# Optimization experiments

Hardware: AMD Instinct MI355X
Metric: run time of the kernel (lower is better)

Reference implementation:

```python
import jax, jax.numpy as jnp
import numpy as np

N, E, B = 8192, 131072, 256
F_ATOM, D, H, HD, L, FC, BINS = 92, 256, 8, 32, 6, 512, 256
VMIN, VMAX = 0.0, 8.0


def layer_norm(x, g, b, eps=1e-5):
    mu = jnp.mean(x, axis=-1, keepdims=True)
    var = jnp.var(x, axis=-1, keepdims=True)
    return (x - mu) * jax.lax.rsqrt(var + eps) * g + b


def silu(x):
    return x * jax.nn.sigmoid(x)


def setup_inputs() -> dict:
    key = jax.random.key(0)
    ks = iter(jax.random.split(key, 80))

    def lin(fan_in, shape):
        return jax.random.normal(next(ks), shape, jnp.float32) / np.sqrt(fan_in)

    inp = {
        'x': jax.random.normal(next(ks), (N, F_ATOM), jnp.float32),
        'edge_attr': jax.random.normal(next(ks), (E, 3), jnp.float32) * 2.0,
        'edge_index': jax.random.randint(next(ks), (2, E), 0, N, dtype=jnp.int32),
        'batch': jnp.sort(jax.random.randint(next(ks), (N,), 0, B, dtype=jnp.int32)),
        # atom_embedding: Linear(92,256) -> LN -> SiLU -> Linear(256,256)
        'aw1': lin(F_ATOM, (F_ATOM, D)), 'ab1': jnp.zeros((D,)),
        'ag1': jnp.ones((D,)), 'abt1': jnp.zeros((D,)),
        'aw2': lin(D, (D, D)), 'ab2': jnp.zeros((D,)),
        # rbf MLP: Linear(256,256) LN SiLU Linear LN SiLU Linear
        'rw1': lin(BINS, (BINS, D)), 'rb1': jnp.zeros((D,)),
        'rg1': jnp.ones((D,)), 'rbt1': jnp.zeros((D,)),
        'rw2': lin(D, (D, D)), 'rb2': jnp.zeros((D,)),
        'rg2': jnp.ones((D,)), 'rbt2': jnp.zeros((D,)),
        'rw3': lin(D, (D, D)), 'rb3': jnp.zeros((D,)),
        # L stacked PrdnetConv (edge-conditioned multi-head graph attention)
        'Wq': lin(D, (L, D, D)), 'bq': jnp.zeros((L, D)),
        'Wk': lin(D, (L, D, D)), 'bk': jnp.zeros((L, D)),
        'Wv': lin(D, (L, D, D)), 'bv': jnp.zeros((L, D)),
        'We': lin(D, (L, D, D)), 'be': jnp.zeros((L, D)),
        'Wo': lin(D, (L, D, D)), 'bo': jnp.zeros((L, D)),
        'lng': jnp.ones((L, D)), 'lnb': jnp.zeros((L, D)),
        # FC head: Linear(256,512) then fc_out Linear(512,1)
        'fw1': lin(D, (D, FC)), 'fb1': jnp.zeros((FC,)),
        'fow': lin(FC, (FC, 1)), 'fob': jnp.zeros((1,)),
    }
    return inp


def _forward(x, edge_attr, edge_index, batch, aw1, ab1, ag1, abt1, aw2, ab2,
             rw1, rb1, rg1, rbt1, rw2, rb2, rg2, rbt2, rw3, rb3,
             Wq, bq, Wk, bk, Wv, bv, We, be, Wo, bo, lng, lnb,
             fw1, fb1, fow, fob):
    # atom embedding (dropout = identity at inference)
    node = silu(layer_norm(x @ aw1 + ab1, ag1, abt1)) @ aw2 + ab2  # [N, D]

    # RBF expansion of edge lengths, then edge MLP
    d = jnp.linalg.norm(edge_attr, axis=1)  # [E]
    centers = jnp.linspace(VMIN, VMAX, BINS)
    gamma = 1.0 / (centers[1] - centers[0]) ** 2
    rbf = jnp.exp(-gamma * (d[:, None] - centers[None, :]) ** 2)  # [E, BINS]
    e = silu(layer_norm(rbf @ rw1 + rb1, rg1, rbt1))
    e = silu(layer_norm(e @ rw2 + rb2, rg2, rbt2))
    e = e @ rw3 + rb3  # [E, D]

    src, dst = edge_index[0], edge_index[1]
    inv_sqrt = 1.0 / np.sqrt(HD)
    for l in range(L):
        res = node
        q = (node @ Wq[l] + bq[l]).reshape(N, H, HD)
        k = (node @ Wk[l] + bk[l]).reshape(N, H, HD)
        v = (node @ Wv[l] + bv[l]).reshape(N, H, HD)
        ee = (e @ We[l] + be[l]).reshape(E, H, HD)
        kj = k[src] + ee  # edge-conditioned keys [E, H, HD]
        vj = v[src] + ee  # edge-conditioned values
        score = jnp.sum(q[dst] * kj, axis=-1) * inv_sqrt  # [E, H]
        smax = jax.ops.segment_max(score, dst, num_segments=N)  # [N, H]
        ex = jnp.exp(score - smax[dst])
        den = jax.ops.segment_sum(ex, dst, num_segments=N)
        alpha = ex / (den[dst] + 1e-16)  # neighborhood softmax [E, H]
        msg = jax.ops.segment_sum(alpha[:, :, None] * vj, dst, num_segments=N)
        out = msg.reshape(N, D) @ Wo[l] + bo[l]
        out = layer_norm(out, lng[l], lnb[l])
        node = out + res  # residual

    # scatter-mean graph pooling
    sums = jax.ops.segment_sum(node, batch, num_segments=B)  # [B, D]
    cnt = jax.ops.segment_sum(jnp.ones((N,), node.dtype), batch, num_segments=B)
    feats = sums / jnp.clip(cnt, 1.0)[:, None]

    feats = feats @ fw1 + fb1  # single fc layer: no act (i == len-1 in source)
    return feats @ fow + fob  # [B, 1], identity link


def reference(x, edge_attr, edge_index, batch, aw1, ab1, ag1, abt1, aw2, ab2,
              rw1, rb1, rg1, rbt1, rw2, rb2, rg2, rbt2, rw3, rb3,
              Wq, bq, Wk, bk, Wv, bv, We, be, Wo, bo, lng, lnb,
              fw1, fb1, fow, fob):
    return _forward(x, edge_attr, edge_index, batch, aw1, ab1, ag1, abt1, aw2,
                    ab2, rw1, rb1, rg1, rbt1, rw2, rb2, rg2, rbt2, rw3, rb3,
                    Wq, bq, Wk, bk, Wv, bv, We, be, Wo, bo, lng, lnb,
                    fw1, fb1, fow, fob)
```

## Files before the change

kernel.cpp:

```cpp
#include <hip/hip_runtime.h>
#include <hip/hip_bf16.h>
#include <cstddef>

#define NN    8192
#define EE    131072
#define BB    256
#define F_AT  92
#define DD    256
#define HH    8
#define HDIM  32
#define LL    6
#define FCD   512

typedef __hip_bfloat16 bf16;
typedef __attribute__((ext_vector_type(8))) __bf16 bf16x8;
typedef __attribute__((ext_vector_type(4))) float f32x4;

__device__ __forceinline__ float to_f(float x) { return x; }
__device__ __forceinline__ float to_f(bf16 x) { return __bfloat162float(x); }
__device__ __forceinline__ float bfu(unsigned short u) {
    return __uint_as_float(((unsigned)u) << 16);
}
__device__ __forceinline__ unsigned short bfbits(float x) {
    bf16 h = __float2bfloat16(x);
    return *(unsigned short*)&h;
}
__device__ __forceinline__ void store_v(float* p, float v) { *p = v; }
__device__ __forceinline__ void store_v(bf16* p, float v) { *p = __float2bfloat16(v); }

__device__ __forceinline__ float4 load4(const float* p) { return *(const float4*)p; }
__device__ __forceinline__ float4 load4(const bf16* p) {
    const ushort4 r = *(const ushort4*)p;
    return make_float4(bfu(r.x), bfu(r.y), bfu(r.z), bfu(r.w));
}

__device__ __forceinline__ void store_f4(float* p, const float4& f) {
    *(float4*)p = f;
}
__device__ __forceinline__ void store_f4(bf16* p, const float4& f) {
    ushort4 u = {bfbits(f.x), bfbits(f.y), bfbits(f.z), bfbits(f.w)};
    *(ushort4*)p = u;
}

__device__ __forceinline__ bf16x8 ld8(const bf16* p) { return *(const bf16x8*)p; }
__device__ __forceinline__ bf16x8 ld8(const float* p) {
    const float4 f0 = *(const float4*)p;
    const float4 f1 = *(const float4*)(p + 4);
    bf16x8 r;
    r[0] = (__bf16)f0.x; r[1] = (__bf16)f0.y; r[2] = (__bf16)f0.z; r[3] = (__bf16)f0.w;
    r[4] = (__bf16)f1.x; r[5] = (__bf16)f1.y; r[6] = (__bf16)f1.z; r[7] = (__bf16)f1.w;
    return r;
}

__device__ __forceinline__ void async_copy16(const void* g, void* l) {
    __builtin_amdgcn_global_load_lds(
        (const __attribute__((address_space(1))) unsigned int*)g,
        (__attribute__((address_space(3))) unsigned int*)l, 16, 0, 0);
}

__global__ __launch_bounds__(256) void transpose_weights(
    const float* __restrict__ rw1, const float* __restrict__ rw2,
    const float* __restrict__ rw3, const float* __restrict__ aw2,
    const float* __restrict__ Wq, const float* __restrict__ Wk,
    const float* __restrict__ Wv, const float* __restrict__ We,
    const float* __restrict__ Wo, __bf16* __restrict__ out)
{
    __shared__ float tile[64][65];
    const int midx = blockIdx.y;
    const float* src;
    if (midx == 0) src = rw1;
    else if (midx == 1) src = rw2;
    else if (midx == 2) src = rw3;
    else if (midx == 3) src = aw2;
    else {
        const int l = (midx - 4) / 5, s = (midx - 4) % 5;
        const float* bases[5] = {Wq, Wk, Wv, We, Wo};
        src = bases[s] + (size_t)l * 65536;
    }
    __bf16* dst = out + (size_t)midx * 65536;
    const int k0 = (blockIdx.x >> 2) * 64;
    const int n0 = (blockIdx.x & 3) * 64;
    const int c = threadIdx.x & 63;
    const int r0 = threadIdx.x >> 6;
#pragma unroll
    for (int p = 0; p < 16; ++p) {
        const int r = r0 + p * 4;
        tile[r][c] = src[(size_t)(k0 + r) * 256 + n0 + c];
    }
    __syncthreads();
#pragma unroll
    for (int p = 0; p < 16; ++p) {
        const int n = r0 + p * 4;
        dst[(size_t)(n0 + n) * 256 + k0 + c] = (__bf16)tile[c][n];
    }
}

__global__ __launch_bounds__(256) void pack_qkv_bias(
    const float* __restrict__ bq, const float* __restrict__ bk,
    const float* __restrict__ bv, float* __restrict__ out)
{
    const int i = blockIdx.x * 256 + threadIdx.x;
    if (i >= LL * 768) return;
    const int l = i / 768, r = i % 768;
    const float* s = (r < 256) ? bq : (r < 512) ? bk : bv;
    out[i] = s[l * 256 + (r & 255)];
}

__global__ __launch_bounds__(256) void combine_w3e(
    const float* __restrict__ rw3, const float* __restrict__ We,
    __bf16* __restrict__ Wt_out)
{
    __shared__ float As[16][65];
    __shared__ float Ws[16][65];
    const int l = blockIdx.z;
    const float* W = We + (size_t)l * 65536;
    __bf16* dst = Wt_out + (size_t)l * 65536;
    const int m0 = blockIdx.x * 64;
    const int n0 = blockIdx.y * 64;
    const int tid = threadIdx.x;
    const int tx = tid & 15, ty = tid >> 4;
    float acc[4][4] = {};

    for (int k0 = 0; k0 < 256; k0 += 16) {
        {
            const int ar = tid >> 2;
            const int ac = (tid & 3) * 4;
#pragma unroll
            for (int j = 0; j < 4; ++j)
                As[ac + j][ar] = rw3[(size_t)(m0 + ar) * 256 + k0 + ac + j];
        }
        {
            const int wr = tid >> 4;
            const int wc = (tid & 15) * 4;
#pragma unroll
            for (int j = 0; j < 4; ++j)
                Ws[wr][wc + j] = W[(size_t)(k0 + wr) * 256 + n0 + wc + j];
        }
        __syncthreads();
#pragma unroll
        for (int kk = 0; kk < 16; ++kk) {
            float a[4], b[4];
#pragma unroll
            for (int i = 0; i < 4; ++i) a[i] = As[kk][ty * 4 + i];
#pragma unroll
            for (int j = 0; j < 4; ++j) b[j] = Ws[kk][tx * 4 + j];
#pragma unroll
            for (int i = 0; i < 4; ++i)
#pragma unroll
                for (int j = 0; j < 4; ++j) acc[i][j] += a[i] * b[j];
        }
        __syncthreads();
    }
#pragma unroll
    for (int i = 0; i < 4; ++i) {
        const int gk = m0 + ty * 4 + i;
#pragma unroll
        for (int j = 0; j < 4; ++j) {
            const int gn = n0 + tx * 4 + j;
            dst[(size_t)gn * 256 + gk] = (__bf16)acc[i][j];
        }
    }
}

__global__ __launch_bounds__(256) void combine_bias(
    const float* __restrict__ rb3, const float* __restrict__ We,
    const float* __restrict__ be, float* __restrict__ out)
{
    const int l = blockIdx.x;
    const int n = threadIdx.x;
    const float* W = We + (size_t)l * 65536;
    float s = be[l * 256 + n];
    for (int m = 0; m < 256; ++m) s += rb3[m] * W[m * 256 + n];
    out[l * 256 + n] = s;
}

__global__ __launch_bounds__(256) void mfma_gemm_ln(
    const bf16* __restrict__ A, const __bf16* __restrict__ Wt,
    const float* __restrict__ bias, const float* __restrict__ g,
    const float* __restrict__ b, bf16* __restrict__ C, int do_silu)
{
    __shared__ __align__(16) __bf16 As[64 * 64];
    __shared__ __align__(16) __bf16 Bs[256 * 64];
    const int tid = threadIdx.x;
    const int m0 = blockIdx.x * 64;
    const int wave = tid >> 6, lane = tid & 63;
    const int lm = lane & 15, lq = lane >> 4;
    const int lrow = lane >> 3;
    const int lcolsw = ((lane & 7) ^ lrow) * 8;

    f32x4 acc[16] = {};

    for (int k0 = 0; k0 < 256; k0 += 64) {
#pragma unroll
        for (int p = 0; p < 2; ++p) {
            const int rbase = wave * 16 + p * 8;
            async_copy16(A + (size_t)(m0 + rbase + lrow) * 256 + k0 + lcolsw,
                         As + rbase * 64);
        }
#pragma unroll
        for (int p = 0; p < 8; ++p) {
            const int rbase = wave * 64 + p * 8;
            async_copy16(Wt + (size_t)(rbase + lrow) * 256 + k0 + lcolsw,
                         Bs + rbase * 64);
        }
        __syncthreads();
#pragma unroll
        for (int ks = 0; ks < 2; ++ks) {
            const int sw = ((ks * 4 + lq) ^ (lm & 7)) * 8;
            const bf16x8 a = *(const bf16x8*)(As + (wave * 16 + lm) * 64 + sw);
#pragma unroll
            for (int j = 0; j < 16; ++j) {
                const bf16x8 bf = *(const bf16x8*)(Bs + (j * 16 + lm) * 64 + sw);
                acc[j] = __builtin_amdgcn_mfma_f32_16x16x32_bf16(a, bf, acc[j], 0, 0, 0);
            }
        }
        __syncthreads();
    }

    float gg[16], bb[16];
#pragma unroll
    for (int j = 0; j < 16; ++j) {
        const float bv = bias[j * 16 + lm];
        gg[j] = g[j * 16 + lm];
        bb[j] = b[j * 16 + lm];
#pragma unroll
        for (int r = 0; r < 4; ++r) acc[j][r] += bv;
    }

#pragma unroll
    for (int r = 0; r < 4; ++r) {
        float s = 0.f, q = 0.f;
#pragma unroll
        for (int j = 0; j < 16; ++j) { const float v = acc[j][r]; s += v; q += v * v; }
#pragma unroll
        for (int msk = 1; msk < 16; msk <<= 1) {
            s += __shfl_xor(s, msk);
            q += __shfl_xor(q, msk);
        }
        const float mean = s * (1.f / 256.f);
        const float var = q * (1.f / 256.f) - mean * mean;
        const float rs = rsqrtf(var + 1e-5f);
        __bf16* erow = Bs + (wave * 16 + lq * 4 + r) * 256;
#pragma unroll
        for (int j = 0; j < 16; ++j) {
            float v = (acc[j][r] - mean) * rs * gg[j] + bb[j];
            if (do_silu) v = v / (1.f + __expf(-v));
            erow[j * 16 + lm] = (__bf16)v;
        }
    }
    __syncthreads();
    {
        __bf16* cbase = (__bf16*)C + (size_t)m0 * 256;
#pragma unroll
        for (int p = 0; p < 8; ++p) {
            const int ofs = (tid + p * 256) * 8;
            *(bf16x8*)(cbase + ofs) = *(const bf16x8*)(Bs + ofs);
        }
    }
}

__global__ __launch_bounds__(256) void mfma_gemm_ee(
    const bf16* __restrict__ A, const __bf16* __restrict__ Wt,
    const float* __restrict__ bias, bf16* __restrict__ C,
    int M, int Nn, int K)
{
    __shared__ __align__(16) __bf16 smem[128 * 128];
    __bf16* As = smem;
    __bf16* Bs = smem + 128 * 64;
    const int tid = threadIdx.x;

    const int nt_n = Nn >> 7;
    const int xcd = blockIdx.x & 7;
    const int local = blockIdx.x >> 3;
    const int per_xcd = (M >> 7) >> 3;
    const int m0 = (xcd * per_xcd + local / nt_n) * 128;
    const int n0 = (local % nt_n) * 128;

    const int wave = tid >> 6, lane = tid & 63;
    const int wm = (wave & 1) * 64, wn = (wave >> 1) * 64;
    const int lm = lane & 15, lq = lane >> 4;
    const int lrow = lane >> 3;
    const int lcolsw = ((lane & 7) ^ lrow) * 8;

    f32x4 acc[4][4] = {};

    for (int k0 = 0; k0 < K; k0 += 64) {
#pragma unroll
        for (int p = 0; p < 4; ++p) {
            const int rbase = wave * 32 + p * 8;
            async_copy16(A  + (size_t)(m0 + rbase + lrow) * K + k0 + lcolsw,
                         As + rbase * 64);
            async_copy16(Wt + (size_t)(n0 + rbase + lrow) * K + k0 + lcolsw,
                         Bs + rbase * 64);
        }
        __syncthreads();
#pragma unroll
        for (int ks = 0; ks < 2; ++ks) {
            const int sw = ((ks * 4 + lq) ^ (lm & 7)) * 8;
            bf16x8 a[4], b[4];
#pragma unroll
            for (int i = 0; i < 4; ++i) {
                a[i] = *(const bf16x8*)(As + (wm + i * 16 + lm) * 64 + sw);
                b[i] = *(const bf16x8*)(Bs + (wn + i * 16 + lm) * 64 + sw);
            }
#pragma unroll
            for (int i = 0; i < 4; ++i)
#pragma unroll
                for (int j = 0; j < 4; ++j)
                    acc[i][j] = __builtin_amdgcn_mfma_f32_16x16x32_bf16(
                        a[i], b[j], acc[i][j], 0, 0, 0);
        }
        __syncthreads();
    }

#pragma unroll
    for (int i = 0; i < 4; ++i) {
        const int rl = wm + i * 16 + lq * 4;
#pragma unroll
        for (int j = 0; j < 4; ++j) {
            const int cl = wn + j * 16 + lm;
            const float bb = bias ? bias[n0 + cl] : 0.f;
#pragma unroll
            for (int r = 0; r < 4; ++r)
                smem[(rl + r) * 128 + cl] = (__bf16)(acc[i][j][r] + bb);
        }
    }
    __syncthreads();
#pragma unroll
    for (int p = 0; p < 8; ++p) {
        const int ch = tid + p * 256;
        const int row = ch >> 4;
        const int col = (ch & 15) * 8;
        *(bf16x8*)((__bf16*)C + (size_t)(m0 + row) * Nn + n0 + col) =
            *(const bf16x8*)(smem + row * 128 + col);
    }
}

template <typename AT, typename CT>
__global__ __launch_bounds__(256) void mfma_gemm(
    const AT* __restrict__ A, const __bf16* __restrict__ Wt,
    const float* __restrict__ bias, CT* __restrict__ C,
    int M, int Nn, int K)
{
    __shared__ __align__(16) __bf16 As[128 * 72];
    __shared__ __align__(16) __bf16 Bs[128 * 72];
    const int tid = threadIdx.x;
    const int m0 = blockIdx.x * 128;
    const int n0 = blockIdx.y * 128;
    const int wave = tid >> 6, lane = tid & 63;
    const int wm = (wave & 1) * 64, wn = (wave >> 1) * 64;
    const int lm = lane & 15, lq = lane >> 4;

    f32x4 acc[4][4] = {};

    const int srow = tid >> 3;
    const int scol = (tid & 7) * 8;

    for (int k0 = 0; k0 < K; k0 += 64) {
#pragma unroll
        for (int p = 0; p < 4; ++p) {
            const int r = srow + 32 * p;
            *(bf16x8*)(As + r * 72 + scol) = ld8(A + (size_t)(m0 + r) * K + k0 + scol);
            *(bf16x8*)(Bs + r * 72 + scol) = *(const bf16x8*)(Wt + (size_t)(n0 + r) * K + k0 + scol);
        }
        __syncthreads();
#pragma unroll
        for (int ks = 0; ks < 2; ++ks) {
            bf16x8 a[4], b[4];
#pragma unroll
            for (int i = 0; i < 4; ++i) {
                a[i] = *(const bf16x8*)(As + (wm + i * 16 + lm) * 72 + ks * 32 + lq * 8);
                b[i] = *(const bf16x8*)(Bs + (wn + i * 16 + lm) * 72 + ks * 32 + lq * 8);
            }
#pragma unroll
            for (int i = 0; i < 4; ++i)
#pragma unroll
                for (int j = 0; j < 4; ++j)
                    acc[i][j] = __builtin_amdgcn_mfma_f32_16x16x32_bf16(
                        a[i], b[j], acc[i][j], 0, 0, 0);
        }
        __syncthreads();
    }

#pragma unroll
    for (int i = 0; i < 4; ++i) {
        const int gm = m0 + wm + i * 16 + lq * 4;
#pragma unroll
        for (int j = 0; j < 4; ++j) {
            const int gn = n0 + wn + j * 16 + lm;
            const float bv = bias ? bias[gn] : 0.f;
#pragma unroll
            for (int r = 0; r < 4; ++r)
                store_v(&C[(size_t)(gm + r) * Nn + gn], acc[i][j][r] + bv);
        }
    }
}

template <typename AT, typename CT>
__global__ __launch_bounds__(256) void gemm_bias(
    const AT* __restrict__ A, const float* __restrict__ W,
    const float* __restrict__ bias, CT* __restrict__ C,
    int M, int Nn, int K)
{
    __shared__ float As[16][65];
    __shared__ float Ws[16][65];
    const int m0 = blockIdx.x * 64;
    const int n0 = blockIdx.y * 64;
    const int tid = threadIdx.x;
    const int tx = tid & 15, ty = tid >> 4;
    float acc[4][4] = {};

    for (int k0 = 0; k0 < K; k0 += 16) {
        {
            const int ar = tid >> 2;
            const int ac = (tid & 3) * 4;
            const int gm = m0 + ar;
#pragma unroll
            for (int j = 0; j < 4; ++j) {
                const int gk = k0 + ac + j;
                float v = 0.f;
                if (gm < M && gk < K) v = to_f(A[(size_t)gm * K + gk]);
                As[ac + j][ar] = v;
            }
        }
        {
            const int wr = tid >> 4;
            const int wc = (tid & 15) * 4;
            const int gk = k0 + wr;
#pragma unroll
            for (int j = 0; j < 4; ++j) {
                float v = 0.f;
                if (gk < K) v = W[(size_t)gk * Nn + n0 + wc + j];
                Ws[wr][wc + j] = v;
            }
        }
        __syncthreads();
#pragma unroll
        for (int kk = 0; kk < 16; ++kk) {
            float a[4], b[4];
#pragma unroll
            for (int i = 0; i < 4; ++i) a[i] = As[kk][ty * 4 + i];
#pragma unroll
            for (int j = 0; j < 4; ++j) b[j] = Ws[kk][tx * 4 + j];
#pragma unroll
            for (int i = 0; i < 4; ++i)
#pragma unroll
                for (int j = 0; j < 4; ++j) acc[i][j] += a[i] * b[j];
        }
        __syncthreads();
    }
#pragma unroll
    for (int i = 0; i < 4; ++i) {
        const int gm = m0 + ty * 4 + i;
        if (gm >= M) continue;
#pragma unroll
        for (int j = 0; j < 4; ++j) {
            const int gn = n0 + tx * 4 + j;
            float v = acc[i][j];
            if (bias) v += bias[gn];
            store_v(&C[(size_t)gm * Nn + gn], v);
        }
    }
}

__global__ __launch_bounds__(256) void rbf_kernel(
    const float* __restrict__ ea, const int* __restrict__ eid,
    bf16* __restrict__ rbf)
{
    const int p = blockIdx.x * 4 + (threadIdx.x >> 6);
    const int e = eid[p];
    const int c0 = (threadIdx.x & 63) * 4;
    const float ax = ea[e * 3 + 0];
    const float ay = ea[e * 3 + 1];
    const float az = ea[e * 3 + 2];
    const float d = sqrtf(ax * ax + ay * ay + az * az);
    const float step = 8.0f / 255.0f;
    const float gamma = 1.0f / (step * step);
    float o[4];
#pragma unroll
    for (int j = 0; j < 4; ++j) {
        const float t = d - (float)(c0 + j) * step;
        o[j] = __expf(-gamma * t * t);
    }
    store_f4(rbf + (size_t)p * DD + c0, make_float4(o[0], o[1], o[2], o[3]));
}

template <typename XT, typename YT>
__global__ __launch_bounds__(256) void ln_act_kernel(
    const XT* __restrict__ X, YT* __restrict__ Y,
    const float* __restrict__ g, const float* __restrict__ b,
    const float* __restrict__ resid, int rows, int do_silu)
{
    const int wave = threadIdx.x >> 6;
    const int lane = threadIdx.x & 63;
    const int r = blockIdx.x * 4 + wave;
    if (r >= rows) return;
    const float4 x = load4(X + (size_t)r * DD + lane * 4);
    float s = x.x + x.y + x.z + x.w;
    float q = x.x * x.x + x.y * x.y + x.z * x.z + x.w * x.w;
    for (int off = 32; off; off >>= 1) {
        s += __shfl_down(s, off);
        q += __shfl_down(q, off);
    }
    s = __shfl(s, 0);
    q = __shfl(q, 0);
    const float mean = s * (1.f / 256.f);
    const float var = q * (1.f / 256.f) - mean * mean;
    const float rs = rsqrtf(var + 1e-5f);
    const int c = lane * 4;
    float xs[4] = {x.x, x.y, x.z, x.w};
    float out[4];
#pragma unroll
    for (int i = 0; i < 4; ++i) {
        float v = (xs[i] - mean) * rs * g[c + i] + b[c + i];
        if (do_silu) v = v / (1.f + __expf(-v));
        out[i] = v;
    }
    if (resid) {
        const float4 rv = load4(resid + (size_t)r * DD + c);
        out[0] += rv.x; out[1] += rv.y; out[2] += rv.z; out[3] += rv.w;
    }
    store_f4(Y + (size_t)r * DD + c, make_float4(out[0], out[1], out[2], out[3]));
}

__global__ __launch_bounds__(256) void deg_kernel(
    const int* __restrict__ dst, int* __restrict__ deg)
{
    const int e = blockIdx.x * 256 + threadIdx.x;
    if (e < EE) atomicAdd(&deg[dst[e]], 1);
}

__global__ __launch_bounds__(256) void csr_scan(
    const int* __restrict__ deg, int* __restrict__ rowptr)
{
    __shared__ int part[256];
    const int t = threadIdx.x;
    int local[32];
    int s = 0;
#pragma unroll
    for (int i = 0; i < 32; ++i) { local[i] = deg[t * 32 + i]; s += local[i]; }
    part[t] = s;
    __syncthreads();
    if (t == 0) {
        int run = 0;
        for (int i = 0; i < 256; ++i) { const int v = part[i]; part[i] = run; run += v; }
    }
    __syncthreads();
    int run = part[t];
#pragma unroll
    for (int i = 0; i < 32; ++i) { rowptr[t * 32 + i] = run; run += local[i]; }
    if (t == 255) rowptr[NN] = run;
}

__global__ __launch_bounds__(256) void fill_kernel(
    const int* __restrict__ src, const int* __restrict__ dst,
    const int* __restrict__ rowptr, int* __restrict__ fill,
    int* __restrict__ eid, int* __restrict__ srcc)
{
    const int e = blockIdx.x * 256 + threadIdx.x;
    if (e >= EE) return;
    const int d = dst[e];
    const int pos = atomicAdd(&fill[d], 1);
    const int q = rowptr[d] + pos;
    eid[q] = e;
    srcc[q] = src[e];
}

__global__ __launch_bounds__(256) void attn_kernel(
    const bf16* __restrict__ qkv, const bf16* __restrict__ ee, int estride,
    const int* __restrict__ rowptr, const int* __restrict__ srcc,
    float* __restrict__ msg)
{
    const int n = blockIdx.x;
    const int tid = threadIdx.x;
    const int wave = tid >> 6, lane = tid & 63;
    const int e0 = rowptr[n];
    const int deg = rowptr[n + 1] - e0;

    if (deg == 0) {
        msg[(size_t)n * DD + tid] = 0.f;
        return;
    }

    __shared__ float wm[4][HH];
    __shared__ float wl[4][HH];
    __shared__ float wacc[4][DD];

    const float4 qreg = load4(qkv + (size_t)n * 768 + lane * 4);

    float m = -3.402823466e38f, l = 0.f;
    float4 acc = {0.f, 0.f, 0.f, 0.f};

    int j = wave;
    float4 kv = {0.f, 0.f, 0.f, 0.f};
    float4 vv = kv, ev = kv;
    if (j < deg) {
        const int e = e0 + j;
        const bf16* srow = qkv + (size_t)srcc[e] * 768;
        kv = load4(srow + 256 + lane * 4);
        vv = load4(srow + 512 + lane * 4);
        ev = load4(ee + (size_t)e * estride + lane * 4);
    }
    while (j < deg) {
        const int jn = j + 4;
        float4 kv2 = {0.f, 0.f, 0.f, 0.f};
        float4 vv2 = kv2, ev2 = kv2;
        if (jn < deg) {
            const int e2 = e0 + jn;
            const bf16* srow2 = qkv + (size_t)srcc[e2] * 768;
            kv2 = load4(srow2 + 256 + lane * 4);
            vv2 = load4(srow2 + 512 + lane * 4);
            ev2 = load4(ee + (size_t)e2 * estride + lane * 4);
        }
        float p = qreg.x * (kv.x + ev.x) + qreg.y * (kv.y + ev.y) +
                  qreg.z * (kv.z + ev.z) + qreg.w * (kv.w + ev.w);
        p += __shfl_down(p, 4);
        p += __shfl_down(p, 2);
        p += __shfl_down(p, 1);
        const float s = __shfl(p, lane & 56) * 0.17677669529663687f;
        const float mnew = fmaxf(m, s);
        const float scale = __expf(m - mnew);
        const float pe = __expf(s - mnew);
        l = l * scale + pe;
        acc.x = acc.x * scale + pe * (vv.x + ev.x);
        acc.y = acc.y * scale + pe * (vv.y + ev.y);
        acc.z = acc.z * scale + pe * (vv.z + ev.z);
        acc.w = acc.w * scale + pe * (vv.w + ev.w);
        m = mnew;
        kv = kv2; vv = vv2; ev = ev2;
        j = jn;
    }

    if ((lane & 7) == 0) { wm[wave][lane >> 3] = m; wl[wave][lane >> 3] = l; }
    *(float4*)(&wacc[wave][lane * 4]) = acc;
    __syncthreads();

    {
        const int c = tid, h = tid >> 5;
        float M = wm[0][h];
#pragma unroll
        for (int i = 1; i < 4; ++i) M = fmaxf(M, wm[i][h]);
        float L = 0.f, num = 0.f;
#pragma unroll
        for (int i = 0; i < 4; ++i) {
            const float sc = __expf(wm[i][h] - M);
            L += wl[i][h] * sc;
            num += wacc[i][c] * sc;
        }
        msg[(size_t)n * DD + c] = num / (L + 1e-16f);
    }
}

__global__ __launch_bounds__(256) void zero_kernel(float* __restrict__ p, int n)
{
    const int i = blockIdx.x * 256 + threadIdx.x;
    if (i < n) p[i] = 0.f;
}

__global__ __launch_bounds__(256) void pool_kernel(
    const float* __restrict__ node, const int* __restrict__ batch,
    float* __restrict__ sums, float* __restrict__ cnt)
{
    const int n = blockIdx.x;
    const int c = threadIdx.x;
    const int b = batch[n];
    atomicAdd(&sums[b * DD + c], node[(size_t)n * DD + c]);
    if (c == 0) atomicAdd(&cnt[b], 1.0f);
}

__global__ __launch_bounds__(256) void pooled_kernel(
    const float* __restrict__ sums, const float* __restrict__ cnt,
    float* __restrict__ pooled)
{
    const int b = blockIdx.x;
    const int c = threadIdx.x;
    float cc = cnt[b];
    if (cc < 1.f) cc = 1.f;
    pooled[b * DD + c] = sums[b * DD + c] / cc;
}

__global__ __launch_bounds__(64) void final_kernel(
    const float* __restrict__ fc, const float* __restrict__ fow,
    const float* __restrict__ fob, float* __restrict__ out)
{
    const int b = blockIdx.x;
    const int lane = threadIdx.x;
    float s = 0.f;
#pragma unroll
    for (int i = lane; i < FCD; i += 64) s += fc[(size_t)b * FCD + i] * fow[i];
    for (int off = 32; off; off >>= 1) s += __shfl_down(s, off);
    if (lane == 0) out[b] = s + fob[0];
}

extern "C" void kernel_launch(void* const* d_in, const int* in_sizes, int n_in,
                              void* d_out, int out_size, void* d_ws,
                              size_t ws_size, hipStream_t stream)
{
    const float* x         = (const float*)d_in[0];
    const float* edge_attr = (const float*)d_in[1];
    const int*   eidx      = (const int*)d_in[2];
    const int*   batch     = (const int*)d_in[3];
    const float* aw1 = (const float*)d_in[4];
    const float* ab1 = (const float*)d_in[5];
    const float* ag1 = (const float*)d_in[6];
    const float* abt1 = (const float*)d_in[7];
    const float* aw2 = (const float*)d_in[8];
    const float* ab2 = (const float*)d_in[9];
    const float* rw1 = (const float*)d_in[10];
    const float* rb1 = (const float*)d_in[11];
    const float* rg1 = (const float*)d_in[12];
    const float* rbt1 = (const float*)d_in[13];
    const float* rw2 = (const float*)d_in[14];
    const float* rb2 = (const float*)d_in[15];
    const float* rg2 = (const float*)d_in[16];
    const float* rbt2 = (const float*)d_in[17];
    const float* rw3 = (const float*)d_in[18];
    const float* rb3 = (const float*)d_in[19];
    const float* Wq = (const float*)d_in[20];
    const float* bq = (const float*)d_in[21];
    const float* Wk = (const float*)d_in[22];
    const float* bk = (const float*)d_in[23];
    const float* Wv = (const float*)d_in[24];
    const float* bv = (const float*)d_in[25];
    const float* We_ = (const float*)d_in[26];
    const float* be_ = (const float*)d_in[27];
    const float* Wo = (const float*)d_in[28];
    const float* bo = (const float*)d_in[29];
    const float* lng = (const float*)d_in[30];
    const float* lnb = (const float*)d_in[31];
    const float* fw1 = (const float*)d_in[32];
    const float* fb1 = (const float*)d_in[33];
    const float* fow = (const float*)d_in[34];
    const float* fob = (const float*)d_in[35];

    const int* src = eidx;
    const int* dst = eidx + EE;

    char* w = (char*)d_ws;
    size_t off = 0;
    auto alloc = [&](size_t bytes) -> void* {
        void* p = w + off;
        off += (bytes + 255) & ~(size_t)255;
        return p;
    };
    bf16* t_buf = (bf16*)alloc((size_t)EE * DD * 2);
    float* node = (float*)alloc((size_t)NN * DD * 4);
    bf16*  qkv  = (bf16*)alloc((size_t)NN * 768 * 2);
    float* msg  = (float*)alloc((size_t)NN * DD * 4);
    float* outb = (float*)alloc((size_t)NN * DD * 4);
    int* deg    = (int*)alloc((size_t)NN * 4);
    int* fillc  = (int*)alloc((size_t)NN * 4);
    int* rowptr = (int*)alloc((size_t)(NN + 1) * 4);
    int* eid    = (int*)alloc((size_t)EE * 4);
    int* srcc   = (int*)alloc((size_t)EE * 4);
    float* sums  = (float*)alloc((size_t)BB * DD * 4);
    float* cnt   = (float*)alloc((size_t)BB * 4);
    float* pooled = (float*)alloc((size_t)BB * DD * 4);
    float* fc    = (float*)alloc((size_t)BB * FCD * 4);
    __bf16* Wt  = (__bf16*)alloc((size_t)40 * 65536 * 2);
    float* qkvb = (float*)alloc((size_t)LL * 768 * 4);
    float* be_c = (float*)alloc((size_t)LL * 256 * 4);

    const size_t avail = (off <= ws_size) ? ws_size - off : 0;
    int G = 1;
    if      (avail >= (size_t)EE * (6 * DD) * 2 + 256) G = 6;
    else if (avail >= (size_t)EE * (3 * DD) * 2 + 256) G = 3;
    else if (avail >= (size_t)EE * (2 * DD) * 2 + 256) G = 2;
    bf16* e_slab = (bf16*)alloc((size_t)EE * (G * DD) * 2);
    (void)n_in; (void)in_sizes; (void)out_size;

    const dim3 blk(256);
    auto WT = [&](int i) -> const __bf16* { return Wt + (size_t)i * 65536; };

    hipLaunchKernelGGL(transpose_weights, dim3(16, 34), blk, 0, stream,
                       rw1, rw2, rw3, aw2, Wq, Wk, Wv, We_, Wo, Wt);
    hipLaunchKernelGGL(combine_w3e, dim3(4, 4, LL), blk, 0, stream, rw3, We_, Wt + (size_t)34 * 65536);
    hipLaunchKernelGGL(combine_bias, dim3(LL), blk, 0, stream, rb3, We_, be_, be_c);
    hipLaunchKernelGGL(pack_qkv_bias, dim3((LL * 768 + 255) / 256), blk, 0, stream, bq, bk, bv, qkvb);
    hipLaunchKernelGGL(zero_kernel, dim3((2 * NN + 255) / 256), blk, 0, stream, (float*)deg, 2 * NN);
    hipLaunchKernelGGL(deg_kernel, dim3(EE / 256), blk, 0, stream, dst, deg);
    hipLaunchKernelGGL(csr_scan, dim3(1), blk, 0, stream, deg, rowptr);
    hipLaunchKernelGGL(fill_kernel, dim3(EE / 256), blk, 0, stream, src, dst, rowptr, fillc, eid, srcc);

    hipLaunchKernelGGL(rbf_kernel, dim3(EE / 4), blk, 0, stream, edge_attr, eid, t_buf);
    hipLaunchKernelGGL(mfma_gemm_ln, dim3(EE / 64), blk, 0, stream, t_buf, WT(0), rb1, rg1, rbt1, e_slab, 1);
    hipLaunchKernelGGL(mfma_gemm_ln, dim3(EE / 64), blk, 0, stream, e_slab, WT(1), rb2, rg2, rbt2, t_buf, 1);

    {
        dim3 gn64(NN / 64, DD / 64);
        hipLaunchKernelGGL((gemm_bias<float, float>), gn64, blk, 0, stream, x, aw1, ab1, outb, NN, DD, F_AT);
        hipLaunchKernelGGL((ln_act_kernel<float, float>), dim3(NN / 4), blk, 0, stream, outb, outb, ag1, abt1, (const float*)nullptr, NN, 1);
        hipLaunchKernelGGL((mfma_gemm<float, float>), dim3(NN / 128, DD / 128), blk, 0, stream, outb, WT(3), ab2, node, NN, DD, DD);
    }

    for (int l = 0; l < LL; ++l) {
        const size_t bo_ = (size_t)l * DD;
        hipLaunchKernelGGL((mfma_gemm<float, bf16>), dim3(NN / 128, 768 / 128), blk, 0, stream,
                           node, WT(4 + 5 * l), qkvb + (size_t)l * 768, qkv, NN, 768, DD);
        if (l % G == 0) {
            const int nblocks = (EE / 128) * ((G * DD) / 128);
            hipLaunchKernelGGL(mfma_gemm_ee, dim3(nblocks), blk, 0, stream,
                               t_buf, WT(34 + l), be_c + (size_t)l * 256, e_slab, EE, G * DD, DD);
        }
        const bf16* ee_l = e_slab + (size_t)(l % G) * DD;
        hipLaunchKernelGGL(attn_kernel, dim3(NN), blk, 0, stream, qkv, ee_l, G * DD, rowptr, srcc, msg);
        hipLaunchKernelGGL((mfma_gemm<float, float>), dim3(NN / 128, DD / 128), blk, 0, stream, msg, WT(8 + 5 * l), bo + bo_, outb, NN, DD, DD);
        hipLaunchKernelGGL((ln_act_kernel<float, float>), dim3(NN / 4), blk, 0, stream, outb, node, lng + bo_, lnb + bo_, node, NN, 0);
    }

    const int PZ = BB * DD + BB;
    hipLaunchKernelGGL(zero_kernel, dim3((PZ + 255) / 256), blk, 0, stream, sums, PZ);
    hipLaunchKernelGGL(pool_kernel, dim3(NN), blk, 0, stream, node, batch, sums, cnt);
    hipLaunchKernelGGL(pooled_kernel, dim3(BB), blk, 0, stream, sums, cnt, pooled);
    {
        dim3 gf(BB / 64, FCD / 64);
        hipLaunchKernelGGL((gemm_bias<float, float>), gf, blk, 0, stream, pooled, fw1, fb1, fc, BB, FCD, DD);
    }
    hipLaunchKernelGGL(final_kernel, dim3(BB), dim3(64), 0, stream, fc, fow, fob, (float*)d_out);
}
```

Measured before the change: 966.8 us.

## Fuse output projection GEMM with LayerNorm and residual add; swizzle ee epilogue smem

Replaces the per-layer Wo GEMM plus separate LayerNorm/residual kernel with one kernel. Each block computes full 256-wide rows for 64 nodes, so the LN reduction happens in registers and the residual is added straight into node. This removes the intermediate outb round trip and one launch per layer. Separately, the edge GEMM epilogue now XOR-swizzles its shared-memory staging to reduce bank conflicts. The fused kernel launches only 128 blocks, which may underuse the GPU.

```diff
diff --git a/kernel.cpp b/kernel.cpp
--- a/kernel.cpp
+++ b/kernel.cpp
@@ -259,6 +259,82 @@
     }
 }
 
+__global__ __launch_bounds__(256) void mfma_gemm_ln_res(
+    const float* __restrict__ A, const __bf16* __restrict__ Wt,
+    const float* __restrict__ bias, const float* __restrict__ g,
+    const float* __restrict__ b, float* __restrict__ node)
+{
+    __shared__ __align__(16) __bf16 As[64 * 72];
+    __shared__ __align__(16) __bf16 Bs[256 * 64];
+    const int tid = threadIdx.x;
+    const int m0 = blockIdx.x * 64;
+    const int wave = tid >> 6, lane = tid & 63;
+    const int lm = lane & 15, lq = lane >> 4;
+    const int lrow = lane >> 3;
+    const int lcolsw = ((lane & 7) ^ lrow) * 8;
+
+    f32x4 acc[16] = {};
+    const int srow = tid >> 3;
+    const int scol = (tid & 7) * 8;
+
+    for (int k0 = 0; k0 < 256; k0 += 64) {
+#pragma unroll
+        for (int p = 0; p < 2; ++p) {
+            const int r = srow + 32 * p;
+            *(bf16x8*)(As + r * 72 + scol) = ld8(A + (size_t)(m0 + r) * 256 + k0 + scol);
+        }
+#pragma unroll
+        for (int p = 0; p < 8; ++p) {
+            const int rbase = wave * 64 + p * 8;
+            async_copy16(Wt + (size_t)(rbase + lrow) * 256 + k0 + lcolsw,
+                         Bs + rbase * 64);
+        }
+        __syncthreads();
+#pragma unroll
+        for (int ks = 0; ks < 2; ++ks) {
+            const int sw = ((ks * 4 + lq) ^ (lm & 7)) * 8;
+            const bf16x8 a = *(const bf16x8*)(As + (wave * 16 + lm) * 72 + ks * 32 + lq * 8);
+#pragma unroll
+            for (int j = 0; j < 16; ++j) {
+                const bf16x8 bf = *(const bf16x8*)(Bs + (j * 16 + lm) * 64 + sw);
+                acc[j] = __builtin_amdgcn_mfma_f32_16x16x32_bf16(a, bf, acc[j], 0, 0, 0);
+            }
+        }
+        __syncthreads();
+    }
+
+    float gg[16], bb[16];
+#pragma unroll
+    for (int j = 0; j < 16; ++j) {
+        const float bv = bias[j * 16 + lm];
+        gg[j] = g[j * 16 + lm];
+        bb[j] = b[j * 16 + lm];
+#pragma unroll
+        for (int r = 0; r < 4; ++r) acc[j][r] += bv;
+    }
+
+#pragma unroll
+    for (int r = 0; r < 4; ++r) {
+        float s = 0.f, q = 0.f;
+#pragma unroll
+        for (int j = 0; j < 16; ++j) { const float v = acc[j][r]; s += v; q += v * v; }
+#pragma unroll
+        for (int msk = 1; msk < 16; msk <<= 1) {
+            s += __shfl_xor(s, msk);
+            q += __shfl_xor(q, msk);
+        }
+        const float mean = s * (1.f / 256.f);
+        const float var = q * (1.f / 256.f) - mean * mean;
+        const float rs = rsqrtf(var + 1e-5f);
+        float* crow = node + (size_t)(m0 + wave * 16 + lq * 4 + r) * 256;
+#pragma unroll
+        for (int j = 0; j < 16; ++j) {
+            const float v = (acc[j][r] - mean) * rs * gg[j] + bb[j];
+            crow[j * 16 + lm] += v;
+        }
+    }
+}
+
 __global__ __launch_bounds__(256) void mfma_gemm_ee(
     const bf16* __restrict__ A, const __bf16* __restrict__ Wt,
     const float* __restrict__ bias, bf16* __restrict__ C,
@@ -321,8 +397,11 @@
             const int cl = wn + j * 16 + lm;
             const float bb = bias ? bias[n0 + cl] : 0.f;
 #pragma unroll
-            for (int r = 0; r < 4; ++r)
-                smem[(rl + r) * 128 + cl] = (__bf16)(acc[i][j][r] + bb);
+            for (int r = 0; r < 4; ++r) {
+                const int row = rl + r;
+                smem[row * 128 + (cl ^ ((row & 7) << 3))] =
+                    (__bf16)(acc[i][j][r] + bb);
+            }
         }
     }
     __syncthreads();
@@ -330,9 +409,10 @@
     for (int p = 0; p < 8; ++p) {
         const int ch = tid + p * 256;
         const int row = ch >> 4;
-        const int col = (ch & 15) * 8;
-        *(bf16x8*)((__bf16*)C + (size_t)(m0 + row) * Nn + n0 + col) =
-            *(const bf16x8*)(smem + row * 128 + col);
+        const int gcol = ch & 15;
+        const int sg = gcol ^ (row & 7);
+        *(bf16x8*)((__bf16*)C + (size_t)(m0 + row) * Nn + n0 + gcol * 8) =
+            *(const bf16x8*)(smem + row * 128 + sg * 8);
     }
 }
 
@@ -804,8 +884,8 @@
         }
         const bf16* ee_l = e_slab + (size_t)(l % G) * DD;
         hipLaunchKernelGGL(attn_kernel, dim3(NN), blk, 0, stream, qkv, ee_l, G * DD, rowptr, srcc, msg);
-        hipLaunchKernelGGL((mfma_gemm<float, float>), dim3(NN / 128, DD / 128), blk, 0, stream, msg, WT(8 + 5 * l), bo + bo_, outb, NN, DD, DD);
-        hipLaunchKernelGGL((ln_act_kernel<float, float>), dim3(NN / 4), blk, 0, stream, outb, node, lng + bo_, lnb + bo_, node, NN, 0);
+        hipLaunchKernelGGL(mfma_gemm_ln_res, dim3(NN / 64), blk, 0, stream,
+                           msg, WT(8 + 5 * l), bo + bo_, lng + bo_, lnb + bo_, node);
     }
 
     const int PZ = BB * DD + BB;
```

After: 956.1 us. About the same (-1.1%).
